# Kernel optimization log

Hardware: AMD Instinct MI355X
Metric: run time of the kernel (lower is better)

Reference implementation:

```python
import jax, jax.numpy as jnp
import numpy as np

NC = 64      # num_channels per whitening group
T = 5        # Newton-Schulz iterations
EPS = 1e-5


def setup_inputs() -> dict:
    key = jax.random.key(0)
    x = jax.random.normal(key, (64, 256, 56, 56), dtype=jnp.float32)
    weight = jnp.ones((1, 256, 1, 1), dtype=jnp.float32)
    bias = jnp.zeros((1, 256, 1, 1), dtype=jnp.float32)
    return {"x": x, "weight": weight, "bias": bias}


def _iternorm_whiten(X):
    B, C, H, W = X.shape
    g = C // NC
    # (g, nc, m) with m = B*H*W, matching X.transpose(0,1).view(g, nc, -1)
    xv = jnp.transpose(X, (1, 0, 2, 3)).reshape(g, NC, -1)
    m = xv.shape[-1]
    mean = xv.mean(-1, keepdims=True)          # (g, nc, 1)
    xc = xv - mean
    I = jnp.eye(NC, dtype=X.dtype)
    # Sigma = eps*I + xc @ xc^T / m   (baddbmm with beta=eps, alpha=1/m)
    Sigma = EPS * I + jnp.einsum('gdm,gem->gde', xc, xc) / m
    rTr = 1.0 / jnp.trace(Sigma, axis1=1, axis2=2)[:, None, None]  # (g,1,1)
    Sn = Sigma * rTr
    P = jnp.broadcast_to(I, (g, NC, NC))
    for _ in range(T):
        P3 = P @ P @ P
        P = 1.5 * P - 0.5 * (P3 @ Sn)
    wm = P * jnp.sqrt(rTr)                     # whitening matrix per group
    xn = wm @ xc                               # (g, nc, m)
    Xn = jnp.transpose(xn.reshape(C, B, H, W), (1, 0, 2, 3))
    return Xn


def reference(x, weight, bias):
    return _iternorm_whiten(x) * weight + bias
```

## Files before the change

### kernel.cpp

```cpp
#include <hip/hip_runtime.h>
#include <hip/hip_bf16.h>


#define B_    64
#define C_    256
#define HW_   3136
#define G_    4
#define NC_   64
#define M_    (B_*HW_)
#define EPS_  1e-5f
#define TIT_  5

#define NGB_  1024
#define PBLK_ 256

typedef __attribute__((ext_vector_type(8))) short  s16x8;
typedef __attribute__((ext_vector_type(4))) float  f32x4;

#define MFMA_(A,Bv,Cc) Cc = __builtin_amdgcn_mfma_f32_16x16x32_bf16(A, Bv, Cc, 0, 0, 0)

__device__ __forceinline__ unsigned short f2bf(float f){
  union{ float f; unsigned int u; } c; c.f = f;
  unsigned int u = c.u;
  u = u + 0x7FFFu + ((u >> 16) & 1u);
  return (unsigned short)(u >> 16);
}
__device__ __forceinline__ float bf2f(unsigned short h){
  union{ unsigned int u; float f; } c; c.u = ((unsigned int)h) << 16;
  return c.f;
}
__device__ __forceinline__ int swz(int off, int row){
  return off ^ ((row & 7) << 4) ^ (((row >> 3) & 3) << 5);
}
__device__ __forceinline__ s16x8 ld_frag(const unsigned short* base, int row, int kbyte){
  return *(const s16x8*)((const char*)base + swz(row*128 + kbyte, row));
}
__device__ __forceinline__ void st_h(unsigned short* base, int row, int col, unsigned short v){
  *(unsigned short*)((char*)base + swz(row*128 + col*2, row)) = v;
}
__device__ __forceinline__ unsigned short ld_h(const unsigned short* base, int row, int col){
  return *(const unsigned short*)((const char*)base + swz(row*128 + col*2, row));
}

template<bool ATOMIC>
__global__ __launch_bounds__(256) void k_gram(const float* __restrict__ x,
                                              float* __restrict__ S1,
                                              float* __restrict__ S2,
                                              float* __restrict__ partS2,
                                              float* __restrict__ partS1){
  __shared__ __align__(16) unsigned short tile[2][64*64];
  const int tid  = threadIdx.x;
  const int lane = tid & 63, wave = tid >> 6;
  const int bx   = blockIdx.x;
  const int g = bx >> 8, sub = bx & 255, b = sub >> 2, quad = sub & 3;
  const int ck0 = (quad*49) >> 2, ck1 = ((quad+1)*49) >> 2;
  const float* xg = x + ((size_t)b*C_ + (size_t)g*NC_) * HW_;
  const int chb = (tid >> 4) * 4;
  const int posoff = (tid & 15) * 4;
  const int wrow = (wave >> 1) * 32, wcol = (wave & 1) * 32;
  float s1a[4] = {0.f,0.f,0.f,0.f};
  f32x4 acc[2][2] = {};
  float v[4][4];

  auto load_c = [&](int ck){
    #pragma unroll
    for(int q = 0; q < 4; ++q){
      const float4 t = *(const float4*)(xg + (size_t)(chb+q)*HW_ + ck*64 + posoff);
      v[q][0]=t.x; v[q][1]=t.y; v[q][2]=t.z; v[q][3]=t.w;
    }
  };
  auto write_c = [&](unsigned short* tl){
    #pragma unroll
    for(int q = 0; q < 4; ++q){
      s1a[q] += v[q][0]+v[q][1]+v[q][2]+v[q][3];
      const int ch = chb + q;
      const unsigned long long pk =
            (unsigned long long)f2bf(v[q][0])
          | ((unsigned long long)f2bf(v[q][1]) << 16)
          | ((unsigned long long)f2bf(v[q][2]) << 32)
          | ((unsigned long long)f2bf(v[q][3]) << 48);
      *(unsigned long long*)((char*)tl + swz(ch*128 + posoff*2, ch)) = pk;
    }
  };
  auto comp = [&](const unsigned short* tl){
    #pragma unroll
    for(int ks = 0; ks < 2; ++ks){
      const int kbyte = ks*64 + (lane >> 4) * 16;
      s16x8 a0 = ld_frag(tl, wrow +      (lane & 15), kbyte);
      s16x8 a1 = ld_frag(tl, wrow + 16 + (lane & 15), kbyte);
      s16x8 b0 = ld_frag(tl, wcol +      (lane & 15), kbyte);
      s16x8 b1 = ld_frag(tl, wcol + 16 + (lane & 15), kbyte);
      MFMA_(a0, b0, acc[0][0]);
      MFMA_(a0, b1, acc[0][1]);
      MFMA_(a1, b0, acc[1][0]);
      MFMA_(a1, b1, acc[1][1]);
    }
  };

  load_c(ck0);
  write_c(tile[0]);
  __syncthreads();
  for(int ck = ck0; ck < ck1; ++ck){
    const int cur = (ck - ck0) & 1;
    const bool more = (ck + 1 < ck1);
    if(more) load_c(ck + 1);
    comp(tile[cur]);
    if(more) write_c(tile[cur ^ 1]);
    __syncthreads();
  }

  if(ATOMIC){
    float* S2g = S2 + g * (NC_*NC_);
    #pragma unroll
    for(int i = 0; i < 2; ++i)
    #pragma unroll
    for(int j = 0; j < 2; ++j)
    #pragma unroll
    for(int r = 0; r < 4; ++r){
      const int d = wrow + 16*i + (lane >> 4)*4 + r;
      const int e = wcol + 16*j + (lane & 15);
      atomicAdd(&S2g[d*NC_ + e], acc[i][j][r]);
    }
  }else{
    float* p2 = partS2 + (size_t)bx*4096 + tid*16;
    #pragma unroll
    for(int i = 0; i < 2; ++i)
    #pragma unroll
    for(int j = 0; j < 2; ++j)
      *(f32x4*)(p2 + (i*2+j)*4) = acc[i][j];
  }
  #pragma unroll
  for(int q = 0; q < 4; ++q){
    float s = s1a[q];
    #pragma unroll
    for(int m2 = 1; m2 < 16; m2 <<= 1) s += __shfl_xor(s, m2, 64);
    if((lane & 15) == 0){
      if(ATOMIC) atomicAdd(&S1[g*NC_ + chb + q], s);
      else       partS1[(size_t)bx*64 + chb + q] = s;
    }
  }
}

__global__ __launch_bounds__(256) void k_reduce(const float* __restrict__ partS2,
                                                const float* __restrict__ partS1,
                                                float* __restrict__ S1,
                                                float* __restrict__ S2){
  const int bid = blockIdx.x, tid = threadIdx.x;
  if(bid < 64){
    const int flat = bid*256 + tid;
    const int g = flat >> 12, t = flat & 4095;
    const float* p = partS2 + (size_t)(g*PBLK_)*4096 + t;
    float s = 0.f;
    for(int jb = 0; jb < PBLK_; ++jb) s += p[(size_t)jb*4096];
    const int tt = t >> 4, q = (t >> 2) & 3, r = t & 3;
    const int wave = tt >> 6, lane = tt & 63;
    const int d = (wave >> 1)*32 + ((q >> 1) << 4) + ((lane >> 4) << 2) + r;
    const int e = (wave &  1)*32 + ((q &  1) << 4) + (lane & 15);
    S2[g*4096 + d*64 + e] = s;
  }else{
    const int g = tid >> 6, ch = tid & 63;
    const float* p = partS1 + (size_t)(g*PBLK_)*64 + ch;
    float s = 0.f;
    for(int jb = 0; jb < PBLK_; ++jb) s += p[(size_t)jb*64];
    S1[tid] = s;
  }
}

__device__ __forceinline__ void mm_core(f32x4 acc[2][2],
    const unsigned short* Ah, const unsigned short* Al,
    const unsigned short* Bh, const unsigned short* Bl,
    int lane, int wrow, int wcol){
  #pragma unroll
  for(int ks = 0; ks < 2; ++ks){
    const int kbyte = ks*64 + (lane >> 4) * 16;
    s16x8 ah0 = ld_frag(Ah, wrow +      (lane & 15), kbyte);
    s16x8 ah1 = ld_frag(Ah, wrow + 16 + (lane & 15), kbyte);
    s16x8 al0 = ld_frag(Al, wrow +      (lane & 15), kbyte);
    s16x8 al1 = ld_frag(Al, wrow + 16 + (lane & 15), kbyte);
    s16x8 bh0 = ld_frag(Bh, wcol +      (lane & 15), kbyte);
    s16x8 bh1 = ld_frag(Bh, wcol + 16 + (lane & 15), kbyte);
    s16x8 bl0 = ld_frag(Bl, wcol +      (lane & 15), kbyte);
    s16x8 bl1 = ld_frag(Bl, wcol + 16 + (lane & 15), kbyte);
    MFMA_(ah0, bh0, acc[0][0]); MFMA_(ah0, bl0, acc[0][0]); MFMA_(al0, bh0, acc[0][0]);
    MFMA_(ah0, bh1, acc[0][1]); MFMA_(ah0, bl1, acc[0][1]); MFMA_(al0, bh1, acc[0][1]);
    MFMA_(ah1, bh0, acc[1][0]); MFMA_(ah1, bl0, acc[1][0]); MFMA_(al1, bh0, acc[1][0]);
    MFMA_(ah1, bh1, acc[1][1]); MFMA_(ah1, bl1, acc[1][1]); MFMA_(al1, bh1, acc[1][1]);
  }
}

__device__ __forceinline__ void mm64(unsigned short* dH, unsigned short* dL,
    const unsigned short* Ah, const unsigned short* Al,
    const unsigned short* Bh, const unsigned short* Bl,
    int lane, int wrow, int wcol){
  f32x4 acc[2][2] = {};
  mm_core(acc, Ah, Al, Bh, Bl, lane, wrow, wcol);
  #pragma unroll
  for(int i = 0; i < 2; ++i)
  #pragma unroll
  for(int j = 0; j < 2; ++j)
  #pragma unroll
  for(int r = 0; r < 4; ++r){
    const int d = wrow + 16*i + (lane >> 4)*4 + r;
    const int e = wcol + 16*j + (lane & 15);
    const float v = acc[i][j][r];
    const unsigned short h = f2bf(v);
    st_h(dH, d, e, h);
    st_h(dL, d, e, f2bf(v - bf2f(h)));
  }
}

__device__ __forceinline__ void ns_update(unsigned short* dH, unsigned short* dL,
    const unsigned short* Zh, const unsigned short* Zl,
    const unsigned short* Snh, const unsigned short* Snl,
    const unsigned short* pH, const unsigned short* pL,
    int lane, int wrow, int wcol){
  f32x4 acc[2][2] = {};
  mm_core(acc, Zh, Zl, Snh, Snl, lane, wrow, wcol);
  #pragma unroll
  for(int i = 0; i < 2; ++i)
  #pragma unroll
  for(int j = 0; j < 2; ++j)
  #pragma unroll
  for(int r = 0; r < 4; ++r){
    const int d = wrow + 16*i + (lane >> 4)*4 + r;
    const int e = wcol + 16*j + (lane & 15);
    const float pv = bf2f(ld_h(pH, d, e)) + bf2f(ld_h(pL, d, e));
    const float v = 1.5f*pv - 0.5f*acc[i][j][r];
    const unsigned short h = f2bf(v);
    st_h(dH, d, e, h);
    st_h(dL, d, e, f2bf(v - bf2f(h)));
  }
}

__global__ __launch_bounds__(256) void k_ns(const float* __restrict__ S1,
                                            const float* __restrict__ S2,
                                            float* __restrict__ wm,
                                            float* __restrict__ mu){
  __shared__ __align__(16) unsigned short smem[8*4096];
  unsigned short* Snh = smem;
  unsigned short* Snl = smem + 1*4096;
  unsigned short* Xh  = smem + 2*4096;
  unsigned short* Xl  = smem + 3*4096;
  unsigned short* Yh  = smem + 4*4096;
  unsigned short* Yl  = smem + 5*4096;
  unsigned short* Zh  = smem + 6*4096;
  unsigned short* Zl  = smem + 7*4096;
  const int g = blockIdx.x, tid = threadIdx.x;
  const int lane = tid & 63, wave = tid >> 6;
  const float* S1g = S1 + g*NC_;
  const float* S2g = S2 + g*NC_*NC_;
  const float invm = 1.0f / (float)M_;

  float tr = 0.f;
  for(int i = 0; i < NC_; ++i){
    const float mui = S1g[i] * invm;
    tr += S2g[i*NC_ + i]*invm - mui*mui + EPS_;
  }
  const float rTr  = 1.0f / tr;
  const float srtr = sqrtf(rTr);

  {
    const int d  = tid >> 2;
    const int e0 = (tid & 3) * 16;
    const float mud = S1g[d] * invm;
    for(int k = 0; k < 16; ++k){
      const int e = e0 + k;
      const float mue = S1g[e] * invm;
      const float s = (S2g[d*NC_ + e]*invm - mud*mue + ((d==e)?EPS_:0.f)) * rTr;
      const unsigned short h = f2bf(s);
      st_h(Snh, d, e, h);
      st_h(Snl, d, e, f2bf(s - bf2f(h)));
      st_h(Xh,  d, e, (d==e)?(unsigned short)0x3F80:(unsigned short)0);
      st_h(Xl,  d, e, (unsigned short)0);
    }
    if(tid < NC_) mu[g*NC_ + tid] = S1g[tid]*invm;
  }
  __syncthreads();

  unsigned short *pH = Xh, *pL = Xl, *qH = Yh, *qL = Yl;
  const int wrow = (wave >> 1)*32, wcol = (wave & 1)*32;
  for(int it = 0; it < TIT_; ++it){
    mm64(qH, qL, pH, pL, pH, pL, lane, wrow, wcol);
    __syncthreads();
    mm64(Zh, Zl, qH, qL, pH, pL, lane, wrow, wcol);
    __syncthreads();
    ns_update(qH, qL, Zh, Zl, Snh, Snl, pH, pL, lane, wrow, wcol);
    __syncthreads();
    unsigned short* t;
    t = pH; pH = qH; qH = t;
    t = pL; pL = qL; qL = t;
  }

  float* wmg = wm + g*NC_*NC_;
  const int d  = tid >> 2;
  const int e0 = (tid & 3) * 16;
  for(int k = 0; k < 16; ++k){
    const int e = e0 + k;
    wmg[d*NC_ + e] = (bf2f(ld_h(pH, d, e)) + bf2f(ld_h(pL, d, e))) * srtr;
  }
}

__global__ __launch_bounds__(256) void k_apply(const float* __restrict__ x,
                                               const float* __restrict__ wm,
                                               const float* __restrict__ mu,
                                               const float* __restrict__ weight,
                                               const float* __restrict__ bias,
                                               float* __restrict__ out){
  __shared__ __align__(16) unsigned short tileT[2][64*64];
  const int tid  = threadIdx.x;
  const int lane = tid & 63, wave = tid >> 6;
  const int bx   = blockIdx.x;
  const int g = bx >> 9, sub = bx & 511, b = sub >> 3, oct = sub & 7;
  const int ck0 = (oct*49) >> 3, ck1 = ((oct+1)*49) >> 3;
  const float* xg = x   + ((size_t)b*C_ + (size_t)g*NC_) * HW_;
  float*       og = out + ((size_t)b*C_ + (size_t)g*NC_) * HW_;
  const int chb = (tid >> 4) * 4;
  const int posoff = (tid & 15) * 4;

  float mu4[4];
  #pragma unroll
  for(int q = 0; q < 4; ++q) mu4[q] = mu[g*NC_ + chb + q];

  const float* wmg = wm + g*NC_*NC_;
  const int arow = wave*16 + (lane & 15);
  s16x8 ah[2], al[2];
  #pragma unroll
  for(int ks = 0; ks < 2; ++ks){
    const int kc = ks*32 + (lane >> 4)*8;
    const float* p = wmg + arow*NC_ + kc;
    #pragma unroll
    for(int j = 0; j < 8; ++j){
      const float w = p[j];
      const unsigned short h = f2bf(w);
      ah[ks][j] = (short)h;
      al[ks][j] = (short)f2bf(w - bf2f(h));
    }
  }
  const int cl = wave*16 + (lane & 15);
  const float wt  = weight[g*NC_ + cl];
  const float bsv = bias  [g*NC_ + cl];

  float v[4][4];
  auto load_c = [&](int ck){
    #pragma unroll
    for(int q = 0; q < 4; ++q){
      const float4 t = *(const float4*)(xg + (size_t)(chb+q)*HW_ + ck*64 + posoff);
      v[q][0]=t.x; v[q][1]=t.y; v[q][2]=t.z; v[q][3]=t.w;
    }
  };
  auto write_c = [&](unsigned short* tl){
    #pragma unroll
    for(int r = 0; r < 4; ++r){
      const int p = posoff + r;
      const unsigned long long pk =
            (unsigned long long)f2bf(v[0][r] - mu4[0])
          | ((unsigned long long)f2bf(v[1][r] - mu4[1]) << 16)
          | ((unsigned long long)f2bf(v[2][r] - mu4[2]) << 32)
          | ((unsigned long long)f2bf(v[3][r] - mu4[3]) << 48);
      *(unsigned long long*)((char*)tl + p*128 + ((chb*2) ^ ((p & 7) << 4))) = pk;
    }
  };
  auto comp = [&](const unsigned short* tl, int p0){
    #pragma unroll
    for(int tn = 0; tn < 4; ++tn){
      f32x4 acc = {0.f,0.f,0.f,0.f};
      const int pos = tn*16 + (lane & 15);
      #pragma unroll
      for(int ks = 0; ks < 2; ++ks){
        const int cb = (ks*64 + (lane >> 4)*16) ^ ((pos & 7) << 4);
        const s16x8 afr = *(const s16x8*)((const char*)tl + pos*128 + cb);
        MFMA_(afr, ah[ks], acc);
        MFMA_(afr, al[ks], acc);
      }
      const int pr = p0 + tn*16 + ((lane >> 4) << 2);
      f32x4 o;
      o[0] = acc[0]*wt + bsv;
      o[1] = acc[1]*wt + bsv;
      o[2] = acc[2]*wt + bsv;
      o[3] = acc[3]*wt + bsv;
      __builtin_nontemporal_store(o, (f32x4*)(og + (size_t)cl*HW_ + pr));
    }
  };

  load_c(ck0);
  write_c(tileT[0]);
  __syncthreads();
  for(int ck = ck0; ck < ck1; ++ck){
    const int cur = (ck - ck0) & 1;
    const bool more = (ck + 1 < ck1);
    if(more) load_c(ck + 1);
    comp(tileT[cur], ck*64);
    if(more) write_c(tileT[cur ^ 1]);
    __syncthreads();
  }
}

extern "C" void kernel_launch(void* const* d_in, const int* in_sizes, int n_in,
                              void* d_out, int out_size, void* d_ws, size_t ws_size,
                              hipStream_t stream){
  (void)in_sizes; (void)n_in; (void)out_size;
  const float* x  = (const float*)d_in[0];
  const float* w  = (const float*)d_in[1];
  const float* bs = (const float*)d_in[2];
  float* out = (float*)d_out;
  float* S1  = (float*)d_ws;
  float* S2  = S1 + 256;
  float* mu  = S2 + G_*NC_*NC_;
  float* wm  = mu + 256;
  float* p2  = wm + G_*NC_*NC_;
  float* p1  = p2 + (size_t)NGB_*4096;
  const size_t need = ((size_t)(256 + G_*4096 + 256 + G_*4096)
                       + (size_t)NGB_*4096 + (size_t)NGB_*64) * sizeof(float);
  if(ws_size >= need){
    k_gram<false><<<NGB_, 256, 0, stream>>>(x, S1, S2, p2, p1);
    k_reduce<<<65, 256, 0, stream>>>(p2, p1, S1, S2);
  }else{
    hipError_t _e = hipMemsetAsync(d_ws, 0, (256 + G_*NC_*NC_)*sizeof(float), stream);
    (void)_e;
    k_gram<true><<<NGB_, 256, 0, stream>>>(x, S1, S2, p2, p1);
  }
  k_ns   <<<G_,   256, 0, stream>>>(S1, S2, wm, mu);
  k_apply<<<2048, 256, 0, stream>>>(x, wm, mu, w, bs, out);
}
```

Before: 160.2 us.

## Fold mean subtraction into per-channel bias and parallelize trace reduction

The per-element mean subtraction in the apply kernel is removed by computing beta = bias - weight * (wm @ mu) once in the Newton-Schulz kernel. The trace sum becomes a wave shuffle reduction instead of a serial loop in every thread, and the apply kernel gets a launch-bounds occupancy hint. The cost is precision: raw x is now rounded to bf16 before centering, so a large mean would add error. The apply kernel is memory-bound, so the saved subtractions may matter little.

Result: slower. 168.6 us (+5.2%).

```diff
diff --git a/kernel.cpp b/kernel.cpp
--- a/kernel.cpp
+++ b/kernel.cpp
@@ -234,8 +234,10 @@
 
 __global__ __launch_bounds__(256) void k_ns(const float* __restrict__ S1,
                                             const float* __restrict__ S2,
+                                            const float* __restrict__ weight,
+                                            const float* __restrict__ bias,
                                             float* __restrict__ wm,
-                                            float* __restrict__ mu){
+                                            float* __restrict__ beta){
   __shared__ __align__(16) unsigned short smem[8*4096];
   unsigned short* Snh = smem;
   unsigned short* Snl = smem + 1*4096;
@@ -251,12 +253,14 @@
   const float* S2g = S2 + g*NC_*NC_;
   const float invm = 1.0f / (float)M_;
 
-  float tr = 0.f;
-  for(int i = 0; i < NC_; ++i){
-    const float mui = S1g[i] * invm;
-    tr += S2g[i*NC_ + i]*invm - mui*mui + EPS_;
-  }
-  const float rTr  = 1.0f / tr;
+  float term;
+  {
+    const float mui = S1g[lane] * invm;
+    term = S2g[lane*NC_ + lane]*invm - mui*mui + EPS_;
+    #pragma unroll
+    for(int m2 = 1; m2 < 64; m2 <<= 1) term += __shfl_xor(term, m2, 64);
+  }
+  const float rTr  = 1.0f / term;
   const float srtr = sqrtf(rTr);
 
   {
@@ -273,7 +277,6 @@
       st_h(Xh,  d, e, (d==e)?(unsigned short)0x3F80:(unsigned short)0);
       st_h(Xl,  d, e, (unsigned short)0);
     }
-    if(tid < NC_) mu[g*NC_ + tid] = S1g[tid]*invm;
   }
   __syncthreads();
 
@@ -294,18 +297,24 @@
   float* wmg = wm + g*NC_*NC_;
   const int d  = tid >> 2;
   const int e0 = (tid & 3) * 16;
+  float rs = 0.f;
   for(int k = 0; k < 16; ++k){
     const int e = e0 + k;
-    wmg[d*NC_ + e] = (bf2f(ld_h(pH, d, e)) + bf2f(ld_h(pL, d, e))) * srtr;
-  }
-}
-
-__global__ __launch_bounds__(256) void k_apply(const float* __restrict__ x,
-                                               const float* __restrict__ wm,
-                                               const float* __restrict__ mu,
-                                               const float* __restrict__ weight,
-                                               const float* __restrict__ bias,
-                                               float* __restrict__ out){
+    const float wv = (bf2f(ld_h(pH, d, e)) + bf2f(ld_h(pL, d, e))) * srtr;
+    wmg[d*NC_ + e] = wv;
+    rs += wv * (S1g[e] * invm);
+  }
+  rs += __shfl_xor(rs, 1, 64);
+  rs += __shfl_xor(rs, 2, 64);
+  if((tid & 3) == 0)
+    beta[g*NC_ + d] = bias[g*NC_ + d] - weight[g*NC_ + d] * rs;
+}
+
+__global__ __launch_bounds__(256, 8) void k_apply(const float* __restrict__ x,
+                                                  const float* __restrict__ wm,
+                                                  const float* __restrict__ beta,
+                                                  const float* __restrict__ weight,
+                                                  float* __restrict__ out){
   __shared__ __align__(16) unsigned short tileT[2][64*64];
   const int tid  = threadIdx.x;
   const int lane = tid & 63, wave = tid >> 6;
@@ -317,10 +326,6 @@
   const int chb = (tid >> 4) * 4;
   const int posoff = (tid & 15) * 4;
 
-  float mu4[4];
-  #pragma unroll
-  for(int q = 0; q < 4; ++q) mu4[q] = mu[g*NC_ + chb + q];
-
   const float* wmg = wm + g*NC_*NC_;
   const int arow = wave*16 + (lane & 15);
   s16x8 ah[2], al[2];
@@ -337,8 +342,8 @@
     }
   }
   const int cl = wave*16 + (lane & 15);
-  const float wt  = weight[g*NC_ + cl];
-  const float bsv = bias  [g*NC_ + cl];
+  const float wt = weight[g*NC_ + cl];
+  const float bt = beta  [g*NC_ + cl];
 
   float v[4][4];
   auto load_c = [&](int ck){
@@ -353,10 +358,10 @@
     for(int r = 0; r < 4; ++r){
       const int p = posoff + r;
       const unsigned long long pk =
-            (unsigned long long)f2bf(v[0][r] - mu4[0])
-          | ((unsigned long long)f2bf(v[1][r] - mu4[1]) << 16)
-          | ((unsigned long long)f2bf(v[2][r] - mu4[2]) << 32)
-          | ((unsigned long long)f2bf(v[3][r] - mu4[3]) << 48);
+            (unsigned long long)f2bf(v[0][r])
+          | ((unsigned long long)f2bf(v[1][r]) << 16)
+          | ((unsigned long long)f2bf(v[2][r]) << 32)
+          | ((unsigned long long)f2bf(v[3][r]) << 48);
       *(unsigned long long*)((char*)tl + p*128 + ((chb*2) ^ ((p & 7) << 4))) = pk;
     }
   };
@@ -374,10 +379,10 @@
       }
       const int pr = p0 + tn*16 + ((lane >> 4) << 2);
       f32x4 o;
-      o[0] = acc[0]*wt + bsv;
-      o[1] = acc[1]*wt + bsv;
-      o[2] = acc[2]*wt + bsv;
-      o[3] = acc[3]*wt + bsv;
+      o[0] = acc[0]*wt + bt;
+      o[1] = acc[1]*wt + bt;
+      o[2] = acc[2]*wt + bt;
+      o[3] = acc[3]*wt + bt;
       __builtin_nontemporal_store(o, (f32x4*)(og + (size_t)cl*HW_ + pr));
     }
   };
@@ -402,13 +407,13 @@
   const float* x  = (const float*)d_in[0];
   const float* w  = (const float*)d_in[1];
   const float* bs = (const float*)d_in[2];
-  float* out = (float*)d_out;
-  float* S1  = (float*)d_ws;
-  float* S2  = S1 + 256;
-  float* mu  = S2 + G_*NC_*NC_;
-  float* wm  = mu + 256;
-  float* p2  = wm + G_*NC_*NC_;
-  float* p1  = p2 + (size_t)NGB_*4096;
+  float* out  = (float*)d_out;
+  float* S1   = (float*)d_ws;
+  float* S2   = S1 + 256;
+  float* beta = S2 + G_*NC_*NC_;
+  float* wm   = beta + 256;
+  float* p2   = wm + G_*NC_*NC_;
+  float* p1   = p2 + (size_t)NGB_*4096;
   const size_t need = ((size_t)(256 + G_*4096 + 256 + G_*4096)
                        + (size_t)NGB_*4096 + (size_t)NGB_*64) * sizeof(float);
   if(ws_size >= need){
@@ -419,6 +424,6 @@
     (void)_e;
     k_gram<true><<<NGB_, 256, 0, stream>>>(x, S1, S2, p2, p1);
   }
-  k_ns   <<<G_,   256, 0, stream>>>(S1, S2, wm, mu);
-  k_apply<<<2048, 256, 0, stream>>>(x, wm, mu, w, bs, out);
-}
+  k_ns   <<<G_,   256, 0, stream>>>(S1, S2, w, bs, wm, beta);
+  k_apply<<<2048, 256, 0, stream>>>(x, wm, beta, w, out);
+}
```
